# Optimization experiments

Measured on AMD Instinct MI355X. Metric: run time of the kernel, lower is better.

## Reference

```python
import jax, jax.numpy as jnp
import numpy as np

B, N, E, DJ, DE = 1024, 400, 128, 128, 128  # batch, nodes, edges, joint dim, edge dim (E must equal DJ and DE for BatchNorm1d on 3D input)
BN_EPS = 1e-5


def setup_inputs() -> dict:
    key = jax.random.key(0)
    ks = jax.random.split(key, 8)
    gout = jax.random.normal(ks[0], (B, N, DJ), dtype=jnp.float32)
    eout = jax.random.normal(ks[1], (B, E, DE), dtype=jnp.float32)
    start_shift = jax.random.uniform(ks[2], (B, E, N), dtype=jnp.float32)
    end_shift = jax.random.uniform(ks[3], (B, E, N), dtype=jnp.float32)
    # Linear params: nn.init.normal_(std=0.001), bias 0
    W1 = 0.001 * jax.random.normal(ks[4], (DJ, 2 * DJ), dtype=jnp.float32)
    b1 = jnp.zeros((DJ,), dtype=jnp.float32)
    W2 = 0.001 * jax.random.normal(ks[5], (DE, DJ), dtype=jnp.float32)
    b2 = jnp.zeros((DE,), dtype=jnp.float32)
    # BatchNorm affine params: weight=1, bias=0
    g1 = jnp.ones((DJ,), dtype=jnp.float32)
    beta1 = jnp.zeros((DJ,), dtype=jnp.float32)
    g2 = jnp.ones((DE,), dtype=jnp.float32)
    beta2 = jnp.zeros((DE,), dtype=jnp.float32)
    return {"gout": gout, "eout": eout, "start_shift": start_shift, "end_shift": end_shift,
            "W1": W1, "b1": b1, "W2": W2, "b2": b2,
            "g1": g1, "beta1": beta1, "g2": g2, "beta2": beta2}


def batchnorm1d(x, gamma, beta):
    # PyTorch BatchNorm1d on 3D input: channels at dim 1, biased variance over dims (0, 2)
    mean = jnp.mean(x, axis=(0, 2), keepdims=True)
    var = jnp.mean(jnp.square(x - mean), axis=(0, 2), keepdims=True)
    xhat = (x - mean) * jax.lax.rsqrt(var + BN_EPS)
    return xhat * gamma[None, :, None] + beta[None, :, None]


def reference(gout, eout, start_shift, end_shift, W1, b1, W2, b2, g1, beta1, g2, beta2):
    # node -> edge gather via dense shift matmuls: [B,E,N] @ [B,N,DJ] -> [B,E,DJ]
    start_nodes = jnp.matmul(start_shift, gout)
    end_nodes = jnp.matmul(end_shift, gout)
    x = jnp.concatenate([start_nodes, end_nodes], axis=2)  # [B, E, 2*DJ]
    h = jnp.einsum('bef,df->bed', x, W1) + b1  # Linear(2*DJ -> DJ)
    h = jax.nn.relu(batchnorm1d(h, g1, beta1))
    h = jnp.einsum('bed,od->beo', h, W2) + b2  # Linear(DJ -> DE)
    res = batchnorm1d(h, g2, beta2)
    return jax.nn.relu(eout + res)
```

## Files before the change

kernel.cpp:

```cpp
#include <hip/hip_runtime.h>
#include <stdint.h>

#define BB 1024
#define NN 400
#define EE 128
#define DD 128
#define NSLOT 64
#define GTS 424

typedef float f32x4 __attribute__((ext_vector_type(4)));
typedef short bf16x8 __attribute__((ext_vector_type(8)));
typedef short bf16x4 __attribute__((ext_vector_type(4)));

__device__ __forceinline__ short f2bf(float f) {
    uint32_t u = __builtin_bit_cast(uint32_t, f);
    u += 0x7fffu + ((u >> 16) & 1u);
    return (short)(u >> 16);
}

__device__ __forceinline__ float bf2f(short s) {
    return __builtin_bit_cast(float, (uint32_t)((uint16_t)s) << 16);
}

__device__ __forceinline__ bf16x8 cvt8(const f32x4 a, const f32x4 b) {
    bf16x8 r;
    r[0] = f2bf(a[0]); r[1] = f2bf(a[1]); r[2] = f2bf(a[2]); r[3] = f2bf(a[3]);
    r[4] = f2bf(b[0]); r[5] = f2bf(b[1]); r[6] = f2bf(b[2]); r[7] = f2bf(b[3]);
    return r;
}

__global__ __launch_bounds__(1024, 1)
void k1_gemm(const float* __restrict__ gout, const float* __restrict__ ss,
             const float* __restrict__ es, const float* __restrict__ W1,
             const float* __restrict__ b1, unsigned short* __restrict__ h,
             float* __restrict__ stats1)
{
    __shared__ short lds[66560];
    short* GT  = lds;
    short* Ps  = lds;
    short* W1s = lds + 32768;

    const int b   = blockIdx.x;
    const int t   = threadIdx.x;
    const int w   = t >> 6;
    const int l   = t & 63;
    const int l15 = l & 15;
    const int l4  = l >> 4;

    const int arow = (w & 7) * 16 + l15;
    const float* abase = ((w < 8) ? ss : es) + ((size_t)b * EE + arow) * NN;
    const int kkoff = l4 * 8;

    f32x4 pa0 = *(const f32x4*)(abase + kkoff);
    f32x4 pa1 = *(const f32x4*)(abase + kkoff + 4);
    f32x4 pb0 = *(const f32x4*)(abase + 32 + kkoff);
    f32x4 pb1 = *(const f32x4*)(abase + 32 + kkoff + 4);

    {
        const int d  = t & 127;
        const int qb = t >> 7;
        const float* gb = gout + (size_t)b * NN * DD + d;
        for (int q = qb; q < 106; q += 8) {
            int k = 4 * q;
            float v0 = 0.f, v1 = 0.f, v2 = 0.f, v3 = 0.f;
            if (k < NN) {
                v0 = gb[(size_t)k * DD];
                v1 = gb[(size_t)(k + 1) * DD];
                v2 = gb[(size_t)(k + 2) * DD];
                v3 = gb[(size_t)(k + 3) * DD];
            }
            uint32_t lo = (uint32_t)(uint16_t)f2bf(v0) | ((uint32_t)(uint16_t)f2bf(v1) << 16);
            uint32_t hi = (uint32_t)(uint16_t)f2bf(v2) | ((uint32_t)(uint16_t)f2bf(v3) << 16);
            *(uint64_t*)&GT[d * GTS + 4 * q] = ((uint64_t)hi << 32) | lo;
        }
    }
    __syncthreads();

    f32x4 acc[8];
#pragma unroll
    for (int cf = 0; cf < 8; ++cf) acc[cf] = f32x4{0.f, 0.f, 0.f, 0.f};

#pragma unroll
    for (int s = 0; s < 13; ++s) {
        bf16x8 a = cvt8(pa0, pa1);
        pa0 = pb0; pa1 = pb1;
        const int sn = s + 2;
        if (sn < 12) {
            pb0 = *(const f32x4*)(abase + sn * 32 + kkoff);
            pb1 = *(const f32x4*)(abase + sn * 32 + kkoff + 4);
        } else if (sn == 12) {
            int kk = 384 + kkoff;
            pb0 = f32x4{0.f, 0.f, 0.f, 0.f};
            pb1 = f32x4{0.f, 0.f, 0.f, 0.f};
            if (kk < NN)     pb0 = *(const f32x4*)(abase + kk);
            if (kk + 4 < NN) pb1 = *(const f32x4*)(abase + kk + 4);
        }
        const int k0 = s * 32;
#pragma unroll
        for (int cf = 0; cf < 8; ++cf) {
            bf16x8 gf = *(const bf16x8*)&GT[(cf * 16 + l15) * GTS + k0 + kkoff];
            acc[cf] = __builtin_amdgcn_mfma_f32_16x16x32_bf16(a, gf, acc[cf], 0, 0, 0);
        }
    }
    __syncthreads();

#pragma unroll
    for (int cf = 0; cf < 8; ++cf)
#pragma unroll
        for (int r = 0; r < 4; ++r) {
            int row = w * 16 + l4 * 4 + r;
            int col = cf * 16 + l15;
            Ps[row * 128 + (((col >> 3) ^ (row & 7)) << 3) + (col & 7)] = f2bf(acc[cf][r]);
        }
    {
        const int j  = t >> 3;
        const int kc = t & 7;
        const float* wp = W1 + (size_t)j * 256 + kc * 32;
        short* dst = &W1s[j * 264 + kc * 32];
#pragma unroll
        for (int i = 0; i < 4; ++i) {
            f32x4 x0 = *(const f32x4*)(wp + i * 8);
            f32x4 x1 = *(const f32x4*)(wp + i * 8 + 4);
            *(bf16x8*)(dst + i * 8) = cvt8(x0, x1);
        }
    }
    __syncthreads();

    const int mt = w >> 1;
    const int jh = w & 1;
    f32x4 acc2[4];
#pragma unroll
    for (int cf = 0; cf < 4; ++cf) acc2[cf] = f32x4{0.f, 0.f, 0.f, 0.f};

#pragma unroll
    for (int kf = 0; kf < 8; ++kf) {
        int roff = (kf >= 4) ? 128 : 0;
        int kcol = (kf & 3) * 32 + l4 * 8;
        int row  = roff + mt * 16 + l15;
        int cb   = kcol >> 3;
        bf16x8 xf = *(const bf16x8*)&Ps[row * 128 + ((cb ^ (row & 7)) << 3)];
#pragma unroll
        for (int cf = 0; cf < 4; ++cf) {
            int j = jh * 64 + cf * 16 + l15;
            bf16x8 wf = *(const bf16x8*)&W1s[j * 264 + kf * 32 + l4 * 8];
            acc2[cf] = __builtin_amdgcn_mfma_f32_16x16x32_bf16(xf, wf, acc2[cf], 0, 0, 0);
        }
    }
    __syncthreads();

    float* red = (float*)lds;
    float s_r[4] = {0.f, 0.f, 0.f, 0.f};
    float q_r[4] = {0.f, 0.f, 0.f, 0.f};
#pragma unroll
    for (int cf = 0; cf < 4; ++cf) {
        float bv = b1[jh * 64 + cf * 16 + l15];
        f32x4 v = acc2[cf] + bv;
#pragma unroll
        for (int r = 0; r < 4; ++r) {
            int e = mt * 16 + l4 * 4 + r;
            h[((size_t)b * EE + e) * DD + jh * 64 + cf * 16 + l15] = (unsigned short)f2bf(v[r]);
            s_r[r] += v[r];
            q_r[r] += v[r] * v[r];
        }
    }
#pragma unroll
    for (int r = 0; r < 4; ++r) {
        float s = s_r[r], q = q_r[r];
        s += __shfl_xor(s, 1); s += __shfl_xor(s, 2); s += __shfl_xor(s, 4); s += __shfl_xor(s, 8);
        q += __shfl_xor(q, 1); q += __shfl_xor(q, 2); q += __shfl_xor(q, 4); q += __shfl_xor(q, 8);
        if (l15 == 0) {
            int e = mt * 16 + l4 * 4 + r;
            red[((e << 1) | jh)]       = s;
            red[256 + ((e << 1) | jh)] = q;
        }
    }
    __syncthreads();
    if (t < 128) {
        float s = red[2 * t] + red[2 * t + 1];
        float q = red[256 + 2 * t] + red[256 + 2 * t + 1];
        int slot = b & (NSLOT - 1);
        atomicAdd(&stats1[slot * 256 + t], s);
        atomicAdd(&stats1[slot * 256 + 128 + t], q);
    }
}

__global__ __launch_bounds__(256, 4)
void k3_gemm(unsigned short* h, const float* __restrict__ W2,
             const float* __restrict__ b2, const float* __restrict__ g1,
             const float* __restrict__ bt1,
             const float* __restrict__ stats1, float* __restrict__ stats2)
{
    __shared__ short Xs[128 * 128];
    __shared__ float sc[128];
    __shared__ float sh[128];
    const int b   = blockIdx.x;
    const int t   = threadIdx.x;
    const int w   = t >> 6;
    const int l15 = t & 15;
    const int l4  = (t >> 4) & 3;

    if (t < 128) {
        float sm = 0.f, sq = 0.f;
#pragma unroll 8
        for (int sl = 0; sl < NSLOT; ++sl) {
            sm += stats1[sl * 256 + t];
            sq += stats1[sl * 256 + 128 + t];
        }
        const float inv_n = 1.0f / (1024.0f * 128.0f);
        float m    = sm * inv_n;
        float var  = sq * inv_n - m * m;
        float rstd = rsqrtf(var + 1e-5f);
        float s    = rstd * g1[t];
        sc[t] = s;
        sh[t] = bt1[t] - m * s;
    }
    __syncthreads();

    {
        const int c8 = t & 15;
        const int eb = t >> 4;
#pragma unroll
        for (int p = 0; p < 8; ++p) {
            int e = eb + 16 * p;
            bf16x8 v8 = *(const bf16x8*)&h[((size_t)b * EE + e) * DD + c8 * 8];
            float s = sc[e], s0 = sh[e];
            bf16x8 o;
#pragma unroll
            for (int i = 0; i < 8; ++i)
                o[i] = f2bf(fmaxf(fmaf(bf2f(v8[i]), s, s0), 0.0f));
            *(bf16x8*)&Xs[e * 128 + ((c8 ^ (e & 7)) << 3)] = o;
        }
    }
    __syncthreads();

    f32x4 acc[8][2];
#pragma unroll
    for (int i = 0; i < 8; ++i) {
        acc[i][0] = f32x4{0.f, 0.f, 0.f, 0.f};
        acc[i][1] = f32x4{0.f, 0.f, 0.f, 0.f};
    }
#pragma unroll
    for (int kf = 0; kf < 4; ++kf) {
        const int k0 = kf * 32;
        const int cb = (k0 >> 3) + l4;
        bf16x8 af[8];
#pragma unroll
        for (int rf = 0; rf < 8; ++rf) {
            int row = rf * 16 + l15;
            af[rf] = *(const bf16x8*)&Xs[row * 128 + ((cb ^ (row & 7)) * 8)];
        }
#pragma unroll
        for (int cf = 0; cf < 2; ++cf) {
            int j = w * 32 + cf * 16 + l15;
            const float* wp = W2 + (size_t)j * 128 + k0 + l4 * 8;
            bf16x8 bfr = cvt8(*(const f32x4*)wp, *(const f32x4*)(wp + 4));
#pragma unroll
            for (int rf = 0; rf < 8; ++rf)
                acc[rf][cf] = __builtin_amdgcn_mfma_f32_16x16x32_bf16(af[rf], bfr, acc[rf][cf], 0, 0, 0);
        }
    }

    __syncthreads();
    float* red = (float*)Xs;
    const float bj0 = b2[w * 32 + l15];
    const float bj1 = b2[w * 32 + 16 + l15];
    const int j0 = w * 32 + l15;
#pragma unroll
    for (int rf = 0; rf < 8; ++rf) {
        f32x4 v0 = acc[rf][0] + bj0;
        f32x4 v1 = acc[rf][1] + bj1;
        int elb = rf * 16 + l4 * 4;
#pragma unroll
        for (int r = 0; r < 4; ++r) {
            unsigned short* op = h + (size_t)(b * EE + elb + r) * DD;
            op[j0]      = (unsigned short)f2bf(v0[r]);
            op[j0 + 16] = (unsigned short)f2bf(v1[r]);
            float s = v0[r] + v1[r];
            float q = v0[r] * v0[r] + v1[r] * v1[r];
            s += __shfl_xor(s, 1); s += __shfl_xor(s, 2); s += __shfl_xor(s, 4); s += __shfl_xor(s, 8);
            q += __shfl_xor(q, 1); q += __shfl_xor(q, 2); q += __shfl_xor(q, 4); q += __shfl_xor(q, 8);
            if (l15 == 0) {
                red[(elb + r) * 4 + w]       = s;
                red[512 + (elb + r) * 4 + w] = q;
            }
        }
    }
    __syncthreads();
    if (t < 128) {
        float s = red[t * 4] + red[t * 4 + 1] + red[t * 4 + 2] + red[t * 4 + 3];
        float q = red[512 + t * 4] + red[512 + t * 4 + 1] + red[512 + t * 4 + 2] + red[512 + t * 4 + 3];
        int slot = b & (NSLOT - 1);
        atomicAdd(&stats2[slot * 256 + t], s);
        atomicAdd(&stats2[slot * 256 + 128 + t], q);
    }
}

__global__ __launch_bounds__(256)
void k5_final(const unsigned short* __restrict__ h2, const float* __restrict__ eout,
              const float* __restrict__ g2, const float* __restrict__ bt2,
              float* __restrict__ out, const float* __restrict__ stats2)
{
    __shared__ float sc[128];
    __shared__ float sh[128];
    const int t = threadIdx.x;
    if (t < 128) {
        float sm = 0.f, sq = 0.f;
#pragma unroll 8
        for (int sl = 0; sl < NSLOT; ++sl) {
            sm += stats2[sl * 256 + t];
            sq += stats2[sl * 256 + 128 + t];
        }
        const float inv_n = 1.0f / (1024.0f * 128.0f);
        float m    = sm * inv_n;
        float var  = sq * inv_n - m * m;
        float rstd = rsqrtf(var + 1e-5f);
        float s    = rstd * g2[t];
        sc[t] = s;
        sh[t] = bt2[t] - m * s;
    }
    __syncthreads();

    const int total8 = BB * EE * DD / 8;
    for (int i8 = blockIdx.x * blockDim.x + t; i8 < total8; i8 += gridDim.x * blockDim.x) {
        int e = (i8 >> 4) & 127;
        bf16x8 v8 = *(const bf16x8*)(h2 + (size_t)i8 * 8);
        f32x4 u0 = *(const f32x4*)(eout + (size_t)i8 * 8);
        f32x4 u1 = *(const f32x4*)(eout + (size_t)i8 * 8 + 4);
        float s = sc[e], s0 = sh[e];
        f32x4 o0, o1;
#pragma unroll
        for (int i = 0; i < 4; ++i) {
            o0[i] = fmaxf(u0[i] + fmaf(bf2f(v8[i]), s, s0), 0.0f);
            o1[i] = fmaxf(u1[i] + fmaf(bf2f(v8[i + 4]), s, s0), 0.0f);
        }
        *(f32x4*)(out + (size_t)i8 * 8)     = o0;
        *(f32x4*)(out + (size_t)i8 * 8 + 4) = o1;
    }
}

extern "C" void kernel_launch(void* const* d_in, const int* in_sizes, int n_in,
                              void* d_out, int out_size, void* d_ws, size_t ws_size,
                              hipStream_t stream)
{
    const float* gout  = (const float*)d_in[0];
    const float* eout  = (const float*)d_in[1];
    const float* ss    = (const float*)d_in[2];
    const float* es    = (const float*)d_in[3];
    const float* W1    = (const float*)d_in[4];
    const float* b1    = (const float*)d_in[5];
    const float* W2    = (const float*)d_in[6];
    const float* b2    = (const float*)d_in[7];
    const float* g1    = (const float*)d_in[8];
    const float* bt1   = (const float*)d_in[9];
    const float* g2    = (const float*)d_in[10];
    const float* bt2   = (const float*)d_in[11];

    float* stats1 = (float*)d_ws;
    float* stats2 = stats1 + NSLOT * 256;
    unsigned short* h = (unsigned short*)(stats2 + NSLOT * 256);
    float* out    = (float*)d_out;

    hipMemsetAsync((void*)stats1, 0, 2 * NSLOT * 256 * sizeof(float), stream);
    k1_gemm<<<dim3(BB), dim3(1024), 0, stream>>>(gout, ss, es, W1, b1, h, stats1);
    k3_gemm<<<dim3(BB), dim3(256), 0, stream>>>(h, W2, b2, g1, bt1, stats1, stats2);
    k5_final<<<dim3(2048), dim3(256), 0, stream>>>(h, eout, g2, bt2, out, stats2);
}
```

Before: 246.9 us.

## Shrink k1 LDS footprint to raise occupancy with split-K staging and 512-thread blocks

Rewrites the first GEMM kernel to use 512 threads per block with each wave computing two 16-row tiles. The transposed gout tile is staged into LDS in two K halves rather than all at once, and W1 fragments are read directly from global memory and converted to bf16 rather than staged in LDS. The projection output is written to LDS in two passes. Together these cut LDS from about 130KB to about 59KB, so several blocks can share a CU and hide memory latency. The cost is extra barriers for the mid-loop restage and repeated global W1 reads and conversions in every wave.

```diff
diff --git a/kernel.cpp b/kernel.cpp
--- a/kernel.cpp
+++ b/kernel.cpp
@@ -6,11 +6,12 @@
 #define EE 128
 #define DD 128
 #define NSLOT 64
-#define GTS 424
+#define GTS2 232
+#define KH0 224
+#define KH1 192
 
 typedef float f32x4 __attribute__((ext_vector_type(4)));
 typedef short bf16x8 __attribute__((ext_vector_type(8)));
-typedef short bf16x4 __attribute__((ext_vector_type(4)));
 
 __device__ __forceinline__ short f2bf(float f) {
     uint32_t u = __builtin_bit_cast(uint32_t, f);
@@ -29,16 +30,15 @@
     return r;
 }
 
-__global__ __launch_bounds__(1024, 1)
+__global__ __launch_bounds__(512, 4)
 void k1_gemm(const float* __restrict__ gout, const float* __restrict__ ss,
              const float* __restrict__ es, const float* __restrict__ W1,
              const float* __restrict__ b1, unsigned short* __restrict__ h,
              float* __restrict__ stats1)
 {
-    __shared__ short lds[66560];
-    short* GT  = lds;
-    short* Ps  = lds;
-    short* W1s = lds + 32768;
+    __shared__ short lds[29696];
+    short* GT = lds;
+    short* Ps = lds;
 
     const int b   = blockIdx.x;
     const int t   = threadIdx.x;
@@ -46,138 +46,162 @@
     const int l   = t & 63;
     const int l15 = l & 15;
     const int l4  = l >> 4;
-
-    const int arow = (w & 7) * 16 + l15;
-    const float* abase = ((w < 8) ? ss : es) + ((size_t)b * EE + arow) * NN;
     const int kkoff = l4 * 8;
 
-    f32x4 pa0 = *(const f32x4*)(abase + kkoff);
-    f32x4 pa1 = *(const f32x4*)(abase + kkoff + 4);
-    f32x4 pb0 = *(const f32x4*)(abase + 32 + kkoff);
-    f32x4 pb1 = *(const f32x4*)(abase + 32 + kkoff + 4);
-
-    {
-        const int d  = t & 127;
+    const float* abase0 = ((w < 4) ? ss : es) + ((size_t)b * EE + (w & 3) * 32 + l15) * NN;
+    const float* abase1 = abase0 + 16 * NN;
+
+    f32x4 c00 = *(const f32x4*)(abase0 + kkoff);
+    f32x4 c01 = *(const f32x4*)(abase0 + kkoff + 4);
+    f32x4 c10 = *(const f32x4*)(abase1 + kkoff);
+    f32x4 c11 = *(const f32x4*)(abase1 + kkoff + 4);
+    f32x4 n00 = *(const f32x4*)(abase0 + 32 + kkoff);
+    f32x4 n01 = *(const f32x4*)(abase0 + 32 + kkoff + 4);
+    f32x4 n10 = *(const f32x4*)(abase1 + 32 + kkoff);
+    f32x4 n11 = *(const f32x4*)(abase1 + 32 + kkoff + 4);
+
+    const float* gb = gout + (size_t)b * NN * DD + (t & 127);
+    auto stage = [&](int koff, int nq) {
         const int qb = t >> 7;
-        const float* gb = gout + (size_t)b * NN * DD + d;
-        for (int q = qb; q < 106; q += 8) {
-            int k = 4 * q;
-            float v0 = 0.f, v1 = 0.f, v2 = 0.f, v3 = 0.f;
-            if (k < NN) {
-                v0 = gb[(size_t)k * DD];
-                v1 = gb[(size_t)(k + 1) * DD];
-                v2 = gb[(size_t)(k + 2) * DD];
-                v3 = gb[(size_t)(k + 3) * DD];
-            }
+        short* row = &GT[(t & 127) * GTS2];
+        for (int q = qb; q < nq; q += 4) {
+            int kg = koff + 4 * q;
+            float v0 = (kg     < NN) ? gb[(size_t)(kg)     * DD] : 0.f;
+            float v1 = (kg + 1 < NN) ? gb[(size_t)(kg + 1) * DD] : 0.f;
+            float v2 = (kg + 2 < NN) ? gb[(size_t)(kg + 2) * DD] : 0.f;
+            float v3 = (kg + 3 < NN) ? gb[(size_t)(kg + 3) * DD] : 0.f;
             uint32_t lo = (uint32_t)(uint16_t)f2bf(v0) | ((uint32_t)(uint16_t)f2bf(v1) << 16);
             uint32_t hi = (uint32_t)(uint16_t)f2bf(v2) | ((uint32_t)(uint16_t)f2bf(v3) << 16);
-            *(uint64_t*)&GT[d * GTS + 4 * q] = ((uint64_t)hi << 32) | lo;
-        }
-    }
-    __syncthreads();
-
-    f32x4 acc[8];
-#pragma unroll
-    for (int cf = 0; cf < 8; ++cf) acc[cf] = f32x4{0.f, 0.f, 0.f, 0.f};
+            *(uint64_t*)&row[4 * q] = ((uint64_t)hi << 32) | lo;
+        }
+    };
+
+    stage(0, KH0 / 4);
+    __syncthreads();
+
+    f32x4 acc[2][8];
+#pragma unroll
+    for (int i = 0; i < 2; ++i)
+#pragma unroll
+        for (int j = 0; j < 8; ++j) acc[i][j] = f32x4{0.f, 0.f, 0.f, 0.f};
 
 #pragma unroll
     for (int s = 0; s < 13; ++s) {
-        bf16x8 a = cvt8(pa0, pa1);
-        pa0 = pb0; pa1 = pb1;
+        if (s == 7) {
+            __syncthreads();
+            stage(KH0, KH1 / 4);
+            __syncthreads();
+        }
+        bf16x8 a0 = cvt8(c00, c01);
+        bf16x8 a1 = cvt8(c10, c11);
+        c00 = n00; c01 = n01; c10 = n10; c11 = n11;
         const int sn = s + 2;
         if (sn < 12) {
-            pb0 = *(const f32x4*)(abase + sn * 32 + kkoff);
-            pb1 = *(const f32x4*)(abase + sn * 32 + kkoff + 4);
+            n00 = *(const f32x4*)(abase0 + sn * 32 + kkoff);
+            n01 = *(const f32x4*)(abase0 + sn * 32 + kkoff + 4);
+            n10 = *(const f32x4*)(abase1 + sn * 32 + kkoff);
+            n11 = *(const f32x4*)(abase1 + sn * 32 + kkoff + 4);
         } else if (sn == 12) {
             int kk = 384 + kkoff;
-            pb0 = f32x4{0.f, 0.f, 0.f, 0.f};
-            pb1 = f32x4{0.f, 0.f, 0.f, 0.f};
-            if (kk < NN)     pb0 = *(const f32x4*)(abase + kk);
-            if (kk + 4 < NN) pb1 = *(const f32x4*)(abase + kk + 4);
-        }
-        const int k0 = s * 32;
-#pragma unroll
-        for (int cf = 0; cf < 8; ++cf) {
-            bf16x8 gf = *(const bf16x8*)&GT[(cf * 16 + l15) * GTS + k0 + kkoff];
-            acc[cf] = __builtin_amdgcn_mfma_f32_16x16x32_bf16(a, gf, acc[cf], 0, 0, 0);
-        }
-    }
-    __syncthreads();
-
-#pragma unroll
-    for (int cf = 0; cf < 8; ++cf)
-#pragma unroll
-        for (int r = 0; r < 4; ++r) {
-            int row = w * 16 + l4 * 4 + r;
-            int col = cf * 16 + l15;
-            Ps[row * 128 + (((col >> 3) ^ (row & 7)) << 3) + (col & 7)] = f2bf(acc[cf][r]);
-        }
-    {
-        const int j  = t >> 3;
-        const int kc = t & 7;
-        const float* wp = W1 + (size_t)j * 256 + kc * 32;
-        short* dst = &W1s[j * 264 + kc * 32];
-#pragma unroll
-        for (int i = 0; i < 4; ++i) {
-            f32x4 x0 = *(const f32x4*)(wp + i * 8);
-            f32x4 x1 = *(const f32x4*)(wp + i * 8 + 4);
-            *(bf16x8*)(dst + i * 8) = cvt8(x0, x1);
+            n00 = n01 = n10 = n11 = f32x4{0.f, 0.f, 0.f, 0.f};
+            if (kk < NN) {
+                n00 = *(const f32x4*)(abase0 + kk);
+                n01 = *(const f32x4*)(abase0 + kk + 4);
+                n10 = *(const f32x4*)(abase1 + kk);
+                n11 = *(const f32x4*)(abase1 + kk + 4);
+            }
+        }
+        const int k0 = (s < 7 ? s * 32 : (s - 7) * 32) + kkoff;
+#pragma unroll
+        for (int cg = 0; cg < 4; ++cg) {
+            bf16x8 gf0 = *(const bf16x8*)&GT[(cg * 32 + l15) * GTS2 + k0];
+            bf16x8 gf1 = *(const bf16x8*)&GT[(cg * 32 + 16 + l15) * GTS2 + k0];
+            acc[0][2 * cg]     = __builtin_amdgcn_mfma_f32_16x16x32_bf16(a0, gf0, acc[0][2 * cg], 0, 0, 0);
+            acc[1][2 * cg]     = __builtin_amdgcn_mfma_f32_16x16x32_bf16(a1, gf0, acc[1][2 * cg], 0, 0, 0);
+            acc[0][2 * cg + 1] = __builtin_amdgcn_mfma_f32_16x16x32_bf16(a0, gf1, acc[0][2 * cg + 1], 0, 0, 0);
+            acc[1][2 * cg + 1] = __builtin_amdgcn_mfma_f32_16x16x32_bf16(a1, gf1, acc[1][2 * cg + 1], 0, 0, 0);
         }
     }
     __syncthreads();
 
     const int mt = w >> 1;
     const int jh = w & 1;
-    f32x4 acc2[4];
-#pragma unroll
-    for (int cf = 0; cf < 4; ++cf) acc2[cf] = f32x4{0.f, 0.f, 0.f, 0.f};
-
-#pragma unroll
-    for (int kf = 0; kf < 8; ++kf) {
-        int roff = (kf >= 4) ? 128 : 0;
-        int kcol = (kf & 3) * 32 + l4 * 8;
-        int row  = roff + mt * 16 + l15;
-        int cb   = kcol >> 3;
-        bf16x8 xf = *(const bf16x8*)&Ps[row * 128 + ((cb ^ (row & 7)) << 3)];
+    f32x4 acc2[2][4];
+#pragma unroll
+    for (int i = 0; i < 2; ++i)
+#pragma unroll
+        for (int j = 0; j < 4; ++j) acc2[i][j] = f32x4{0.f, 0.f, 0.f, 0.f};
+
+#pragma unroll
+    for (int pass = 0; pass < 2; ++pass) {
+        if ((pass == 0) == (w < 4)) {
+#pragma unroll
+            for (int rf = 0; rf < 2; ++rf)
+#pragma unroll
+                for (int cf = 0; cf < 8; ++cf)
+#pragma unroll
+                    for (int r = 0; r < 4; ++r) {
+                        int row = (w & 3) * 32 + rf * 16 + l4 * 4 + r;
+                        int col = cf * 16 + l15;
+                        Ps[row * 128 + (((col >> 3) ^ (row & 7)) << 3) + (col & 7)] = f2bf(acc[rf][cf][r]);
+                    }
+        }
+        __syncthreads();
+#pragma unroll
+        for (int kf = 0; kf < 4; ++kf) {
+            bf16x8 xf[2];
+#pragma unroll
+            for (int rf2 = 0; rf2 < 2; ++rf2) {
+                int row = mt * 32 + rf2 * 16 + l15;
+                int cb  = kf * 4 + l4;
+                xf[rf2] = *(const bf16x8*)&Ps[row * 128 + ((cb ^ (row & 7)) << 3)];
+            }
+#pragma unroll
+            for (int cf = 0; cf < 4; ++cf) {
+                int j = jh * 64 + cf * 16 + l15;
+                const float* wp = W1 + (size_t)j * 256 + pass * 128 + kf * 32 + l4 * 8;
+                bf16x8 wf = cvt8(*(const f32x4*)wp, *(const f32x4*)(wp + 4));
+                acc2[0][cf] = __builtin_amdgcn_mfma_f32_16x16x32_bf16(xf[0], wf, acc2[0][cf], 0, 0, 0);
+                acc2[1][cf] = __builtin_amdgcn_mfma_f32_16x16x32_bf16(xf[1], wf, acc2[1][cf], 0, 0, 0);
+            }
+        }
+        __syncthreads();
+    }
+
+    float* red = (float*)lds;
+    float s_r[2][4] = {{0.f,0.f,0.f,0.f},{0.f,0.f,0.f,0.f}};
+    float q_r[2][4] = {{0.f,0.f,0.f,0.f},{0.f,0.f,0.f,0.f}};
+#pragma unroll
+    for (int rf2 = 0; rf2 < 2; ++rf2)
 #pragma unroll
         for (int cf = 0; cf < 4; ++cf) {
-            int j = jh * 64 + cf * 16 + l15;
-            bf16x8 wf = *(const bf16x8*)&W1s[j * 264 + kf * 32 + l4 * 8];
-            acc2[cf] = __builtin_amdgcn_mfma_f32_16x16x32_bf16(xf, wf, acc2[cf], 0, 0, 0);
-        }
-    }
-    __syncthreads();
-
-    float* red = (float*)lds;
-    float s_r[4] = {0.f, 0.f, 0.f, 0.f};
-    float q_r[4] = {0.f, 0.f, 0.f, 0.f};
-#pragma unroll
-    for (int cf = 0; cf < 4; ++cf) {
-        float bv = b1[jh * 64 + cf * 16 + l15];
-        f32x4 v = acc2[cf] + bv;
+            float bv = b1[jh * 64 + cf * 16 + l15];
+            f32x4 v = acc2[rf2][cf] + bv;
+#pragma unroll
+            for (int r = 0; r < 4; ++r) {
+                int e = mt * 32 + rf2 * 16 + l4 * 4 + r;
+                h[((size_t)b * EE + e) * DD + jh * 64 + cf * 16 + l15] = (unsigned short)f2bf(v[r]);
+                s_r[rf2][r] += v[r];
+                q_r[rf2][r] += v[r] * v[r];
+            }
+        }
+#pragma unroll
+    for (int rf2 = 0; rf2 < 2; ++rf2)
 #pragma unroll
         for (int r = 0; r < 4; ++r) {
-            int e = mt * 16 + l4 * 4 + r;
-            h[((size_t)b * EE + e) * DD + jh * 64 + cf * 16 + l15] = (unsigned short)f2bf(v[r]);
-            s_r[r] += v[r];
-            q_r[r] += v[r] * v[r];
-        }
-    }
-#pragma unroll
-    for (int r = 0; r < 4; ++r) {
-        float s = s_r[r], q = q_r[r];
-        s += __shfl_xor(s, 1); s += __shfl_xor(s, 2); s += __shfl_xor(s, 4); s += __shfl_xor(s, 8);
-        q += __shfl_xor(q, 1); q += __shfl_xor(q, 2); q += __shfl_xor(q, 4); q += __shfl_xor(q, 8);
-        if (l15 == 0) {
-            int e = mt * 16 + l4 * 4 + r;
-            red[((e << 1) | jh)]       = s;
-            red[256 + ((e << 1) | jh)] = q;
-        }
-    }
+            float s = s_r[rf2][r], q = q_r[rf2][r];
+            s += __shfl_xor(s, 1); s += __shfl_xor(s, 2); s += __shfl_xor(s, 4); s += __shfl_xor(s, 8);
+            q += __shfl_xor(q, 1); q += __shfl_xor(q, 2); q += __shfl_xor(q, 4); q += __shfl_xor(q, 8);
+            if (l15 == 0) {
+                int e = mt * 32 + rf2 * 16 + l4 * 4 + r;
+                red[(e << 1) | jh]       = s;
+                red[512 + ((e << 1) | jh)] = q;
+            }
+        }
     __syncthreads();
     if (t < 128) {
         float s = red[2 * t] + red[2 * t + 1];
-        float q = red[256 + 2 * t] + red[256 + 2 * t + 1];
+        float q = red[512 + 2 * t] + red[512 + 2 * t + 1];
         int slot = b & (NSLOT - 1);
         atomicAdd(&stats1[slot * 256 + t], s);
         atomicAdd(&stats1[slot * 256 + 128 + t], q);
@@ -361,7 +385,7 @@
     float* out    = (float*)d_out;
 
     hipMemsetAsync((void*)stats1, 0, 2 * NSLOT * 256 * sizeof(float), stream);
-    k1_gemm<<<dim3(BB), dim3(1024), 0, stream>>>(gout, ss, es, W1, b1, h, stats1);
+    k1_gemm<<<dim3(BB), dim3(512), 0, stream>>>(gout, ss, es, W1, b1, h, stats1);
     k3_gemm<<<dim3(BB), dim3(256), 0, stream>>>(h, W2, b2, g1, bt1, stats1, stats2);
     k5_final<<<dim3(2048), dim3(256), 0, stream>>>(h, eout, g2, bt2, out, stats2);
 }
```

New measurement: 328.3 us. +33.0%, slower.

## Split gout staging into K halves and pre-convert weights to bf16

Applied to the files above, without the earlier changes.

Stages the transposed gout tile in two K halves with a smaller LDS buffer and removes the W1 LDS copy. This shrinks shared memory per block so more blocks can be resident per CU. A new small kernel converts W1 and W2 to bf16 once per call, so k1 and k3 read bf16 weights directly from global memory instead of converting them per block. The cost is extra barriers mid-loop, uncached-in-LDS weight reads, and one more kernel launch.

```diff
diff --git a/kernel.cpp b/kernel.cpp
--- a/kernel.cpp
+++ b/kernel.cpp
@@ -6,11 +6,12 @@
 #define EE 128
 #define DD 128
 #define NSLOT 64
-#define GTS 424
+#define GTS2 232
+#define KH0 224
+#define KH1 192
 
 typedef float f32x4 __attribute__((ext_vector_type(4)));
 typedef short bf16x8 __attribute__((ext_vector_type(8)));
-typedef short bf16x4 __attribute__((ext_vector_type(4)));
 
 __device__ __forceinline__ short f2bf(float f) {
     uint32_t u = __builtin_bit_cast(uint32_t, f);
@@ -29,16 +30,24 @@
     return r;
 }
 
-__global__ __launch_bounds__(1024, 1)
+__global__ __launch_bounds__(256)
+void k0_cvtw(const float* __restrict__ W1, const float* __restrict__ W2,
+             unsigned short* __restrict__ W1b, unsigned short* __restrict__ W2b)
+{
+    int i = blockIdx.x * 256 + threadIdx.x;
+    if (i < 32768) W1b[i] = (unsigned short)f2bf(W1[i]);
+    if (i < 16384) W2b[i] = (unsigned short)f2bf(W2[i]);
+}
+
+__global__ __launch_bounds__(1024, 8)
 void k1_gemm(const float* __restrict__ gout, const float* __restrict__ ss,
-             const float* __restrict__ es, const float* __restrict__ W1,
+             const float* __restrict__ es, const unsigned short* __restrict__ W1b,
              const float* __restrict__ b1, unsigned short* __restrict__ h,
              float* __restrict__ stats1)
 {
-    __shared__ short lds[66560];
-    short* GT  = lds;
-    short* Ps  = lds;
-    short* W1s = lds + 32768;
+    __shared__ short lds[32768];
+    short* GT = lds;
+    short* Ps = lds;
 
     const int b   = blockIdx.x;
     const int t   = threadIdx.x;
@@ -46,34 +55,33 @@
     const int l   = t & 63;
     const int l15 = l & 15;
     const int l4  = l >> 4;
+    const int kkoff = l4 * 8;
 
     const int arow = (w & 7) * 16 + l15;
     const float* abase = ((w < 8) ? ss : es) + ((size_t)b * EE + arow) * NN;
-    const int kkoff = l4 * 8;
 
     f32x4 pa0 = *(const f32x4*)(abase + kkoff);
     f32x4 pa1 = *(const f32x4*)(abase + kkoff + 4);
     f32x4 pb0 = *(const f32x4*)(abase + 32 + kkoff);
     f32x4 pb1 = *(const f32x4*)(abase + 32 + kkoff + 4);
 
-    {
-        const int d  = t & 127;
+    const float* gb = gout + (size_t)b * NN * DD + (t & 127);
+    auto stage = [&](int koff, int nq) {
         const int qb = t >> 7;
-        const float* gb = gout + (size_t)b * NN * DD + d;
-        for (int q = qb; q < 106; q += 8) {
-            int k = 4 * q;
-            float v0 = 0.f, v1 = 0.f, v2 = 0.f, v3 = 0.f;
-            if (k < NN) {
-                v0 = gb[(size_t)k * DD];
-                v1 = gb[(size_t)(k + 1) * DD];
-                v2 = gb[(size_t)(k + 2) * DD];
-                v3 = gb[(size_t)(k + 3) * DD];
-            }
+        short* row = &GT[(t & 127) * GTS2];
+        for (int q = qb; q < nq; q += 8) {
+            int kg = koff + 4 * q;
+            float v0 = (kg     < NN) ? gb[(size_t)(kg)     * DD] : 0.f;
+            float v1 = (kg + 1 < NN) ? gb[(size_t)(kg + 1) * DD] : 0.f;
+            float v2 = (kg + 2 < NN) ? gb[(size_t)(kg + 2) * DD] : 0.f;
+            float v3 = (kg + 3 < NN) ? gb[(size_t)(kg + 3) * DD] : 0.f;
             uint32_t lo = (uint32_t)(uint16_t)f2bf(v0) | ((uint32_t)(uint16_t)f2bf(v1) << 16);
             uint32_t hi = (uint32_t)(uint16_t)f2bf(v2) | ((uint32_t)(uint16_t)f2bf(v3) << 16);
-            *(uint64_t*)&GT[d * GTS + 4 * q] = ((uint64_t)hi << 32) | lo;
-        }
-    }
+            *(uint64_t*)&row[4 * q] = ((uint64_t)hi << 32) | lo;
+        }
+    };
+
+    stage(0, KH0 / 4);
     __syncthreads();
 
     f32x4 acc[8];
@@ -82,6 +90,11 @@
 
 #pragma unroll
     for (int s = 0; s < 13; ++s) {
+        if (s == 7) {
+            __syncthreads();
+            stage(KH0, KH1 / 4);
+            __syncthreads();
+        }
         bf16x8 a = cvt8(pa0, pa1);
         pa0 = pb0; pa1 = pb1;
         const int sn = s + 2;
@@ -95,10 +108,10 @@
             if (kk < NN)     pb0 = *(const f32x4*)(abase + kk);
             if (kk + 4 < NN) pb1 = *(const f32x4*)(abase + kk + 4);
         }
-        const int k0 = s * 32;
+        const int k0 = (s < 7 ? s * 32 : (s - 7) * 32) + kkoff;
 #pragma unroll
         for (int cf = 0; cf < 8; ++cf) {
-            bf16x8 gf = *(const bf16x8*)&GT[(cf * 16 + l15) * GTS + k0 + kkoff];
+            bf16x8 gf = *(const bf16x8*)&GT[(cf * 16 + l15) * GTS2 + k0];
             acc[cf] = __builtin_amdgcn_mfma_f32_16x16x32_bf16(a, gf, acc[cf], 0, 0, 0);
         }
     }
@@ -112,18 +125,6 @@
             int col = cf * 16 + l15;
             Ps[row * 128 + (((col >> 3) ^ (row & 7)) << 3) + (col & 7)] = f2bf(acc[cf][r]);
         }
-    {
-        const int j  = t >> 3;
-        const int kc = t & 7;
-        const float* wp = W1 + (size_t)j * 256 + kc * 32;
-        short* dst = &W1s[j * 264 + kc * 32];
-#pragma unroll
-        for (int i = 0; i < 4; ++i) {
-            f32x4 x0 = *(const f32x4*)(wp + i * 8);
-            f32x4 x1 = *(const f32x4*)(wp + i * 8 + 4);
-            *(bf16x8*)(dst + i * 8) = cvt8(x0, x1);
-        }
-    }
     __syncthreads();
 
     const int mt = w >> 1;
@@ -142,7 +143,7 @@
 #pragma unroll
         for (int cf = 0; cf < 4; ++cf) {
             int j = jh * 64 + cf * 16 + l15;
-            bf16x8 wf = *(const bf16x8*)&W1s[j * 264 + kf * 32 + l4 * 8];
+            bf16x8 wf = *(const bf16x8*)&W1b[(size_t)j * 256 + kf * 32 + l4 * 8];
             acc2[cf] = __builtin_amdgcn_mfma_f32_16x16x32_bf16(xf, wf, acc2[cf], 0, 0, 0);
         }
     }
@@ -170,7 +171,7 @@
         q += __shfl_xor(q, 1); q += __shfl_xor(q, 2); q += __shfl_xor(q, 4); q += __shfl_xor(q, 8);
         if (l15 == 0) {
             int e = mt * 16 + l4 * 4 + r;
-            red[((e << 1) | jh)]       = s;
+            red[(e << 1) | jh]         = s;
             red[256 + ((e << 1) | jh)] = q;
         }
     }
@@ -185,7 +186,7 @@
 }
 
 __global__ __launch_bounds__(256, 4)
-void k3_gemm(unsigned short* h, const float* __restrict__ W2,
+void k3_gemm(unsigned short* h, const unsigned short* __restrict__ W2b,
              const float* __restrict__ b2, const float* __restrict__ g1,
              const float* __restrict__ bt1,
              const float* __restrict__ stats1, float* __restrict__ stats2)
@@ -252,8 +253,7 @@
 #pragma unroll
         for (int cf = 0; cf < 2; ++cf) {
             int j = w * 32 + cf * 16 + l15;
-            const float* wp = W2 + (size_t)j * 128 + k0 + l4 * 8;
-            bf16x8 bfr = cvt8(*(const f32x4*)wp, *(const f32x4*)(wp + 4));
+            bf16x8 bfr = *(const bf16x8*)&W2b[(size_t)j * 128 + k0 + l4 * 8];
 #pragma unroll
             for (int rf = 0; rf < 8; ++rf)
                 acc[rf][cf] = __builtin_amdgcn_mfma_f32_16x16x32_bf16(af[rf], bfr, acc[rf][cf], 0, 0, 0);
@@ -357,11 +357,14 @@
 
     float* stats1 = (float*)d_ws;
     float* stats2 = stats1 + NSLOT * 256;
-    unsigned short* h = (unsigned short*)(stats2 + NSLOT * 256);
+    unsigned short* W1b = (unsigned short*)(stats2 + NSLOT * 256);
+    unsigned short* W2b = W1b + 32768;
+    unsigned short* h   = W2b + 16384;
     float* out    = (float*)d_out;
 
     hipMemsetAsync((void*)stats1, 0, 2 * NSLOT * 256 * sizeof(float), stream);
-    k1_gemm<<<dim3(BB), dim3(1024), 0, stream>>>(gout, ss, es, W1, b1, h, stats1);
-    k3_gemm<<<dim3(BB), dim3(256), 0, stream>>>(h, W2, b2, g1, bt1, stats1, stats2);
+    k0_cvtw<<<dim3(128), dim3(256), 0, stream>>>(W1, W2, W1b, W2b);
+    k1_gemm<<<dim3(BB), dim3(1024), 0, stream>>>(gout, ss, es, W1b, b1, h, stats1);
+    k3_gemm<<<dim3(BB), dim3(256), 0, stream>>>(h, W2b, b2, g1, bt1, stats1, stats2);
     k5_final<<<dim3(2048), dim3(256), 0, stream>>>(h, eout, g2, bt2, out, stats2);
 }
```

Measured after the change: 272.8 us. +10.5%, slower.
